# Kernel optimization log

Measured on AMD Instinct MI355X. Metric: run time of the kernel, lower is better.

## Reference

```python
import jax, jax.numpy as jnp
import numpy as np

B, HIST, N, E = 16, 24, 256, 4096
AQI_EM, RNN_H, GNN_H, EDGE_H = 16, 64, 64, 2


def _lstm(x, W_ih, W_hh, b_ih, b_hh):
    # x: [Bn, L, in]; PyTorch LSTM cell, gate order i,f,g,o
    Bn, L, _ = x.shape
    H = W_hh.shape[1]
    xg = jnp.einsum('bli,gi->blg', x, W_ih) + b_ih  # precompute input contributions [Bn,L,4H]

    def step(carry, g_t):
        h, c = carry
        gates = g_t + h @ W_hh.T + b_hh
        i, f, g, o = jnp.split(gates, 4, axis=-1)
        c = jax.nn.sigmoid(f) * c + jax.nn.sigmoid(i) * jnp.tanh(g)
        h = jax.nn.sigmoid(o) * jnp.tanh(c)
        return (h, c), h

    init = (jnp.zeros((Bn, H), x.dtype), jnp.zeros((Bn, H), x.dtype))
    _, hs = jax.lax.scan(step, init, jnp.swapaxes(xg, 0, 1))
    return jnp.swapaxes(hs, 0, 1)  # [Bn,L,H]


def setup_inputs() -> dict:
    key = jax.random.key(0)
    ks = jax.random.split(key, 8)
    return {
        'city_aqi': jax.random.normal(ks[0], (B, HIST, N, 1), jnp.float32),
        'city_conn': jax.random.randint(ks[1], (2, E), 0, N, jnp.int32),
        'city_w': jax.random.normal(ks[2], (E, EDGE_H), jnp.float32),
        'embed_W': jax.random.normal(ks[3], (1, AQI_EM), jnp.float32) * 0.5,
        'embed_b': jnp.zeros((AQI_EM,), jnp.float32),
        'W_ih': jax.random.normal(ks[4], (4 * RNN_H, AQI_EM), jnp.float32) * (1.0 / np.sqrt(RNN_H)),
        'W_hh': jax.random.normal(ks[5], (4 * RNN_H, RNN_H), jnp.float32) * (1.0 / np.sqrt(RNN_H)),
        'b_ih': jnp.zeros((4 * RNN_H,), jnp.float32),
        'b_hh': jnp.zeros((4 * RNN_H,), jnp.float32),
        'mlp1_W': jax.random.normal(ks[6], (2 * RNN_H + EDGE_H, GNN_H), jnp.float32) * (1.0 / np.sqrt(2 * RNN_H + EDGE_H)),
        'mlp1_b': jnp.zeros((GNN_H,), jnp.float32),
        'mlp2_W': jax.random.normal(ks[7], (RNN_H + GNN_H, GNN_H), jnp.float32) * (1.0 / np.sqrt(RNN_H + GNN_H)),
        'mlp2_b': jnp.zeros((GNN_H,), jnp.float32),
        'city_num': N,
    }


def reference(city_aqi, city_conn, city_w, embed_W, embed_b, W_ih, W_hh, b_ih, b_hh, mlp1_W, mlp1_b, mlp2_W, mlp2_b, city_num):
    Bq, L, Nn, _ = city_aqi.shape
    # embedding + LSTM front-end
    x = jnp.transpose(city_aqi, (0, 2, 1, 3))          # [B,N,L,1]
    x = x @ embed_W + embed_b                          # [B,N,L,em]
    x = x.reshape(Bq * Nn, L, -1)
    h = _lstm(x, W_ih, W_hh, b_ih, b_hh)               # [B*N,L,H]
    h = jnp.transpose(h.reshape(Bq, Nn, L, -1), (0, 2, 1, 3))  # [B,L,N,H]
    # batched graph: T = B*L independent graphs with identical edge structure
    T = Bq * L
    x_flat = h.reshape(T * Nn, -1)                     # [T*N,H]
    off = jnp.arange(T, dtype=city_conn.dtype) * jnp.asarray(city_num, city_conn.dtype)
    row = (city_conn[0][None, :] + off[:, None]).reshape(-1)  # [T*E]
    col = (city_conn[1][None, :] + off[:, None]).reshape(-1)
    e = city_conn.shape[1]
    edge_attr = jnp.broadcast_to(city_w[None], (T, e, city_w.shape[1])).reshape(T * e, -1)
    # CityGNN: gather -> concat -> Linear -> scatter_mean -> concat -> Linear
    msg = jnp.concatenate([x_flat[row], x_flat[col], edge_attr], axis=1)
    msg = msg @ mlp1_W + mlp1_b                        # [T*E,gnn_h]
    agg = jax.ops.segment_sum(msg, col, num_segments=T * Nn)
    cnt = jax.ops.segment_sum(jnp.ones((T * e,), msg.dtype), col, num_segments=T * Nn)
    agg = agg / jnp.maximum(cnt, 1.0)[:, None]         # scatter_mean semantics
    out = jnp.concatenate([x_flat, agg], axis=1) @ mlp2_W + mlp2_b
    return out.reshape(-1, L, Nn, out.shape[-1])       # [B,hist_len,N,gnn_h]
```

## Files before the change

### kernel.cpp

```cpp
#include <hip/hip_runtime.h>
#include <hip/hip_bf16.h>

#define B_ 16
#define L_ 24
#define N_ 256
#define E_ 4096
#define T_ (B_ * L_)

constexpr int WP    = 0;
constexpr int WRQ   = WP + 4096;
constexpr int WRM   = WRQ + 4096;
constexpr int WBIAS = WRM + 4096;
constexpr int WALPHA= WBIAS + 16384;
constexpr int WBETA = WALPHA + 256;
constexpr int WDINV = WBETA + 256;
constexpr int WSEL  = WDINV + 256;
constexpr int WSW   = WSEL + 256;
constexpr int WCNTF = WSW + 512;
constexpr int WCOLP = WCNTF + 256;
constexpr int WROWS = WCOLP + 260;
constexpr int WHFRAG= WROWS + 4096;
constexpr int WQFRAG= WHFRAG + 8192;
constexpr int WX    = WQFRAG + 4096;
constexpr int WAFRG = WX + 3145728;

using bf16x8 = __attribute__((ext_vector_type(8))) short;
using f32x4  = __attribute__((ext_vector_type(4))) float;

__device__ __forceinline__ float sigm(float x) { return 1.f / (1.f + __expf(-x)); }
__device__ __forceinline__ float tanh_(float x) { return 2.f / (1.f + __expf(-2.f * x)) - 1.f; }
__device__ __forceinline__ unsigned f2bf(float f) {
    unsigned u = __float_as_uint(f);
    return (u + 0x7fffu + ((u >> 16) & 1u)) >> 16;
}

__global__ __launch_bounds__(256) void k_prep(
    const int* __restrict__ conn, const float* __restrict__ cw,
    const float* __restrict__ Wih, const float* __restrict__ embW,
    const float* __restrict__ embB, const float* __restrict__ bih,
    const float* __restrict__ bhh, const float* __restrict__ Whh,
    const float* __restrict__ m1W, const float* __restrict__ m1b,
    const float* __restrict__ m2W, const float* __restrict__ m2b,
    float* __restrict__ ws) {
    int t = threadIdx.x, blk = blockIdx.x;
    if (blk >= 9) {
        __shared__ unsigned Mw[256 * 64];
        for (int i = t; i < 256 * 64; i += 256) Mw[i] = 0u;
        __syncthreads();
        for (int e = t; e < E_; e += 256) {
            int k = conn[e] & 255;
            int v = conn[E_ + e] & 255;
            atomicAdd(&Mw[v * 64 + (k >> 2)], 1u << ((k & 3) * 8));
        }
        __syncthreads();
        uint4* dst = (uint4*)(ws + WAFRG);
        int base = (blk - 9) * 2048;
        #pragma unroll
        for (int u0 = 0; u0 < 8; ++u0) {
            int u = base + u0 * 256 + t;
            int fi = u >> 6, l = u & 63;
            int nt = fi >> 3, ks = fi & 7;
            int v = nt * 16 + (l & 15);
            int kb = ks * 8 + ((l >> 4) << 1);
            unsigned w0 = Mw[v * 64 + kb];
            unsigned w1 = Mw[v * 64 + kb + 1];
            unsigned uu[4];
            #pragma unroll
            for (int q = 0; q < 2; ++q) {
                unsigned c0 = (w0 >> (q * 16)) & 255u;
                unsigned c1 = (w0 >> (q * 16 + 8)) & 255u;
                uu[q] = f2bf((float)c0) | (f2bf((float)c1) << 16);
                unsigned d0 = (w1 >> (q * 16)) & 255u;
                unsigned d1 = (w1 >> (q * 16 + 8)) & 255u;
                uu[2 + q] = f2bf((float)d0) | (f2bf((float)d1) << 16);
            }
            dst[u] = make_uint4(uu[0], uu[1], uu[2], uu[3]);
        }
        return;
    }
    if (blk >= 5) {
        int idx = (blk - 5) * 256 + t;
        for (int f = idx; f < 2048; f += 1024) {
            int p = f >> 6, l = f & 63;
            int ct = p >> 1, ks = p & 1;
            const float* src = Whh + (ct * 16 + (l & 15)) * 64 + ks * 32 + ((l >> 4) << 3);
            unsigned u[4];
            #pragma unroll
            for (int q = 0; q < 4; ++q)
                u[q] = f2bf(src[2 * q]) | (f2bf(src[2 * q + 1]) << 16);
            ((uint4*)(ws + WHFRAG))[f] = make_uint4(u[0], u[1], u[2], u[3]);
        }
        return;
    }
    if (blk > 0) {
        __shared__ float sB[64 * 64];
        __shared__ float sM[32 * 64];
        int mi = blk - 1;
        bool isP = mi < 2;
        int ks = mi & 1;
        #pragma unroll
        for (int i = 0; i < 16; ++i) sB[t + 256 * i] = m2W[64 * 64 + t + 256 * i];
        __syncthreads();
        int j = t & 63, kl = t >> 6;
        for (int r = 0; r < 8; ++r) {
            int kk = kl * 8 + r;
            int k = ks * 32 + kk;
            const float* arow = m1W + (isP ? k : (64 + k)) * 64;
            float acc = 0.f;
            #pragma unroll
            for (int m = 0; m < 64; m += 4) {
                float4 a4 = *(const float4*)(arow + m);
                acc = fmaf(a4.x, sB[m * 64 + j], acc);
                acc = fmaf(a4.y, sB[(m + 1) * 64 + j], acc);
                acc = fmaf(a4.z, sB[(m + 2) * 64 + j], acc);
                acc = fmaf(a4.w, sB[(m + 3) * 64 + j], acc);
            }
            if (isP) {
                sM[kk * 64 + j] = acc;
            } else {
                ws[WRM + k * 64 + j] = acc;
                sM[kk * 64 + j] = acc + m2W[k * 64 + j];
            }
        }
        __syncthreads();
        {
            int ct = t >> 6, l = t & 63;
            int fi = (isP ? 8 : 0) + ks * 4 + ct;
            int rb = (l >> 4) * 8;
            int n = ct * 16 + (l & 15);
            unsigned uu[4];
            #pragma unroll
            for (int q = 0; q < 4; ++q)
                uu[q] = f2bf(sM[(rb + 2 * q) * 64 + n])
                      | (f2bf(sM[(rb + 2 * q + 1) * 64 + n]) << 16);
            ((uint4*)(ws + WQFRAG))[fi * 64 + l] = make_uint4(uu[0], uu[1], uu[2], uu[3]);
        }
        return;
    }
    __shared__ int s_cnt[N_];
    __shared__ float s_sw0[N_], s_sw1[N_];
    __shared__ float sU[3 * 64];
    s_cnt[t] = 0; s_sw0[t] = 0.f; s_sw1[t] = 0.f;
    __syncthreads();
    for (int e = t; e < E_; e += 256) {
        int c = conn[E_ + e] & 255;
        atomicAdd(&s_cnt[c], 1);
        atomicAdd(&s_sw0[c], cw[2 * e]);
        atomicAdd(&s_sw1[c], cw[2 * e + 1]);
    }
    __syncthreads();
    int cnt = s_cnt[t];
    ws[WCNTF + t] = (float)cnt;
    ws[WDINV + t] = 1.f / (float)(cnt > 1 ? cnt : 1);
    ws[WSEL + t]  = cnt > 0 ? 1.f : 0.f;
    ws[WSW + t]        = s_sw0[t];
    ws[WSW + N_ + t]   = s_sw1[t];
    float a = 0.f, b = 0.f;
    #pragma unroll
    for (int i = 0; i < 16; ++i) {
        float w = Wih[t * 16 + i];
        a += w * embW[i];
        b += w * embB[i];
    }
    ws[WALPHA + t] = a;
    ws[WBETA + t]  = b + bih[t] + bhh[t];
    if (t < 192) {
        int part = t >> 6, j = t & 63;
        float acc = 0.f;
        #pragma unroll 8
        for (int m = 0; m < 64; ++m) {
            float w = (part == 0) ? m1W[128 * 64 + m]
                    : (part == 1) ? m1W[129 * 64 + m] : m1b[m];
            acc = fmaf(w, m2W[(64 + m) * 64 + j], acc);
        }
        sU[part * 64 + j] = acc;
    }
    __syncthreads();
    {
        int j = t & 63;
        float u0 = sU[j], u1 = sU[64 + j], u2 = sU[128 + j];
        float b2j = m2b[j];
        int vb = t >> 6;
        #pragma unroll 8
        for (int i = 0; i < 64; ++i) {
            int v = vb + i * 4;
            int cv = s_cnt[v];
            float dv = 1.f / (float)(cv > 1 ? cv : 1);
            float bb = s_sw0[v] * u0 + s_sw1[v] * u1 + (float)cv * u2;
            ws[WBIAS + v * 64 + j] = dv * bb + b2j;
        }
    }
}

constexpr int HS = 72;

__global__ __launch_bounds__(256, 1) void k_lstm(
    const float* __restrict__ aqi, float* __restrict__ ws) {
    __shared__ __align__(16) short sHhi[2][16 * HS];
    __shared__ __align__(16) short sHlo[2][16 * HS];
    __shared__ float sX[24 * 16];
    int t = threadIdx.x;
    int w = t >> 6, lane = t & 63;
    int seq0 = blockIdx.x * 16;
    int b0 = seq0 >> 8, n0 = seq0 & 255;
    bf16x8 wreg[4][2];
    {
        const bf16x8* wf = (const bf16x8*)(ws + WHFRAG);
        #pragma unroll
        for (int g = 0; g < 4; ++g)
            #pragma unroll
            for (int ks = 0; ks < 2; ++ks)
                wreg[g][ks] = wf[((4 * g + w) * 2 + ks) * 64 + lane];
    }
    for (int i = t; i < 384; i += 256) {
        int l = i >> 4, c = i & 15;
        sX[l * 16 + c] = aqi[(b0 * L_ + l) * N_ + n0 + c];
    }
    unsigned short* xws = (unsigned short*)(ws + WX);
    int c0 = lane & 15, quad = lane >> 4, q4 = quad * 4, q8 = quad * 8;
    float alF[4], beF[4];
    #pragma unroll
    for (int g = 0; g < 4; ++g) {
        alF[g] = ws[WALPHA + (4 * g + w) * 16 + c0];
        beF[g] = ws[WBETA  + (4 * g + w) * 16 + c0];
    }
    float cst[4] = {0.f, 0.f, 0.f, 0.f};
    bf16x8 hA[2][2] = {};
    __syncthreads();
    for (int l = 0; l < L_; ++l) {
        int buf = l & 1;
        f32x4 acc[4];
        #pragma unroll
        for (int g = 0; g < 4; ++g) {
            #pragma unroll
            for (int r = 0; r < 4; ++r)
                acc[g][r] = fmaf(sX[l * 16 + q4 + r], alF[g], beF[g]);
        }
        if (l > 0) {
            #pragma unroll
            for (int g = 0; g < 4; ++g) {
                #pragma unroll
                for (int ks = 0; ks < 2; ++ks) {
                    acc[g] = __builtin_amdgcn_mfma_f32_16x16x32_bf16(
                        hA[0][ks], wreg[g][ks], acc[g], 0, 0, 0);
                    acc[g] = __builtin_amdgcn_mfma_f32_16x16x32_bf16(
                        hA[1][ks], wreg[g][ks], acc[g], 0, 0, 0);
                }
            }
        }
        unsigned short* xrow = xws + ((size_t)(b0 * L_ + l) * N_ + n0) * 64;
        #pragma unroll
        for (int r = 0; r < 4; ++r) {
            float iv = sigm(acc[0][r]);
            float fv = sigm(acc[1][r]);
            float gv = tanh_(acc[2][r]);
            float ov = sigm(acc[3][r]);
            cst[r] = fmaf(fv, cst[r], iv * gv);
            float h = ov * tanh_(cst[r]);
            unsigned hb = f2bf(h);
            xrow[(q4 + r) * 64 + w * 16 + c0] = (unsigned short)hb;
            float hf = __uint_as_float(hb << 16);
            unsigned lb = f2bf(h - hf);
            sHhi[buf][(q4 + r) * HS + w * 16 + c0] = (short)hb;
            sHlo[buf][(q4 + r) * HS + w * 16 + c0] = (short)lb;
        }
        __syncthreads();
        hA[0][0] = *(const bf16x8*)&sHhi[buf][c0 * HS + q8];
        hA[0][1] = *(const bf16x8*)&sHhi[buf][c0 * HS + 32 + q8];
        hA[1][0] = *(const bf16x8*)&sHlo[buf][c0 * HS + q8];
        hA[1][1] = *(const bf16x8*)&sHlo[buf][c0 * HS + 32 + q8];
    }
}

constexpr int XS = 72;

__global__ __launch_bounds__(256, 2) void k_graph(
    const float* __restrict__ ws, float* __restrict__ out) {
    __shared__ __align__(16) short Xl[N_ * XS];
    __shared__ __align__(16) short Sl[N_ * XS];
    int tg = blockIdx.x;
    int tid = threadIdx.x;
    int lane = tid & 63, w = tid >> 6;
    int c0 = lane & 15, quad = lane >> 4, q8 = quad * 8;
    const uint4* src = (const uint4*)((const unsigned short*)(ws + WX)
                                      + (size_t)tg * (N_ * 64));
    #pragma unroll
    for (int it = 0; it < 8; ++it) {
        int idx = tid + it * 256;
        uint4 d = src[idx];
        int node = idx >> 3, q = idx & 7;
        *(uint4*)&Xl[node * XS + q * 8] = d;
    }
    float dv[16];
    #pragma unroll
    for (int nt = 0; nt < 16; ++nt) dv[nt] = ws[WDINV + nt * 16 + c0];
    __syncthreads();
    bf16x8 af[8];
    {
        int colb = w * 16 + (c0 & 14);
        int sh = (c0 & 1) * 16;
        int rbase = (lane >> 4) * 8;
        #pragma unroll
        for (int ks = 0; ks < 8; ++ks) {
            unsigned wd[8];
            #pragma unroll
            for (int j = 0; j < 8; ++j)
                wd[j] = *(const unsigned*)&Xl[(ks * 32 + rbase + j) * XS + colb];
            union { bf16x8 v; unsigned u[4]; } tmp;
            #pragma unroll
            for (int q = 0; q < 4; ++q)
                tmp.u[q] = ((wd[2 * q] >> sh) & 0xffffu)
                         | (((wd[2 * q + 1] >> sh) & 0xffffu) << 16);
            af[ks] = tmp.v;
        }
    }
    f32x4 acc[16];
    #pragma unroll
    for (int nt = 0; nt < 16; ++nt) {
        #pragma unroll
        for (int r = 0; r < 4; ++r) acc[nt][r] = 0.f;
    }
    {
        const bf16x8* bsrc = (const bf16x8*)(ws + WAFRG);
        #pragma unroll
        for (int nt = 0; nt < 16; ++nt) {
            bf16x8 bf[8];
            #pragma unroll
            for (int ks = 0; ks < 8; ++ks)
                bf[ks] = bsrc[(nt * 8 + ks) * 64 + lane];
            #pragma unroll
            for (int ks = 0; ks < 8; ++ks)
                acc[nt] = __builtin_amdgcn_mfma_f32_16x16x32_bf16(
                    af[ks], bf[ks], acc[nt], 0, 0, 0);
        }
    }
    {
        int j0 = w * 16 + quad * 4;
        #pragma unroll
        for (int nt = 0; nt < 16; ++nt) {
            float d = dv[nt];
            unsigned p0 = f2bf(acc[nt][0] * d) | (f2bf(acc[nt][1] * d) << 16);
            unsigned p1 = f2bf(acc[nt][2] * d) | (f2bf(acc[nt][3] * d) << 16);
            int v = nt * 16 + c0;
            *(uint2*)&Sl[v * XS + j0] = make_uint2(p0, p1);
        }
    }
    __syncthreads();
    bf16x8 bq[16];
    {
        const bf16x8* qf = (const bf16x8*)(ws + WQFRAG);
        #pragma unroll
        for (int i = 0; i < 16; ++i) bq[i] = qf[i * 64 + lane];
    }
    const float* bias = ws + WBIAS;
    #pragma unroll
    for (int rti = 0; rti < 4; ++rti) {
        int rt = w * 4 + rti;
        const short* xr = &Xl[(rt * 16 + c0) * XS];
        const short* sr = &Sl[(rt * 16 + c0) * XS];
        bf16x8 ax0 = *(const bf16x8*)(xr + q8);
        bf16x8 ax1 = *(const bf16x8*)(xr + 32 + q8);
        bf16x8 as0 = *(const bf16x8*)(sr + q8);
        bf16x8 as1 = *(const bf16x8*)(sr + 32 + q8);
        #pragma unroll
        for (int ct = 0; ct < 4; ++ct) {
            f32x4 a2;
            #pragma unroll
            for (int r = 0; r < 4; ++r)
                a2[r] = bias[(rt * 16 + quad * 4 + r) * 64 + ct * 16 + c0];
            a2 = __builtin_amdgcn_mfma_f32_16x16x32_bf16(ax0, bq[ct],      a2, 0, 0, 0);
            a2 = __builtin_amdgcn_mfma_f32_16x16x32_bf16(ax1, bq[4 + ct],  a2, 0, 0, 0);
            a2 = __builtin_amdgcn_mfma_f32_16x16x32_bf16(as0, bq[8 + ct],  a2, 0, 0, 0);
            a2 = __builtin_amdgcn_mfma_f32_16x16x32_bf16(as1, bq[12 + ct], a2, 0, 0, 0);
            #pragma unroll
            for (int r = 0; r < 4; ++r)
                out[((size_t)tg * 256 + rt * 16 + quad * 4 + r) * 64 + ct * 16 + c0]
                    = a2[r];
        }
    }
    int v = tid;
    float sel = ws[WSEL + v];
    if (__syncthreads_or(sel < 0.5f)) {
        if (sel < 0.5f) {
            float* og = out + ((size_t)tg * 256 + v) * 64;
            #pragma unroll
            for (int jc = 0; jc < 4; ++jc) {
                float corr[16];
                #pragma unroll
                for (int j = 0; j < 16; ++j) corr[j] = 0.f;
                #pragma unroll
                for (int k = 0; k < 64; ++k) {
                    unsigned hv = (unsigned short)Xl[v * XS + k];
                    float xk = __uint_as_float(hv << 16);
                    const float* Q = ws + WRM + k * 64 + jc * 16;
                    #pragma unroll
                    for (int j = 0; j < 16; ++j) corr[j] += xk * Q[j];
                }
                #pragma unroll
                for (int j = 0; j < 16; ++j) og[jc * 16 + j] -= corr[j];
            }
        }
    }
}

extern "C" void kernel_launch(void* const* d_in, const int* in_sizes, int n_in,
                              void* d_out, int out_size, void* d_ws, size_t ws_size,
                              hipStream_t stream) {
    const float* aqi  = (const float*)d_in[0];
    const int*   conn = (const int*)d_in[1];
    const float* cw   = (const float*)d_in[2];
    const float* embW = (const float*)d_in[3];
    const float* embB = (const float*)d_in[4];
    const float* Wih  = (const float*)d_in[5];
    const float* Whh  = (const float*)d_in[6];
    const float* bih  = (const float*)d_in[7];
    const float* bhh  = (const float*)d_in[8];
    const float* m1W  = (const float*)d_in[9];
    const float* m1b  = (const float*)d_in[10];
    const float* m2W  = (const float*)d_in[11];
    const float* m2b  = (const float*)d_in[12];
    float* ws  = (float*)d_ws;
    float* out = (float*)d_out;

    k_prep<<<dim3(13), dim3(256), 0, stream>>>(conn, cw, Wih, embW, embB, bih, bhh,
                                               Whh, m1W, m1b, m2W, m2b, ws);
    k_lstm<<<dim3(256), dim3(256), 0, stream>>>(aqi, ws);
    k_graph<<<dim3(T_), dim3(256), 0, stream>>>(ws, out);
}
```

Measured before the change: 158.7 us.

## Merge prep and LSTM kernels into one launch with per-block W_hh conversion

The prep kernel and the LSTM kernel become one launch. Blocks 0-255 run the LSTM and each converts W_hh to bf16 fragments and computes the embedding-folded input weights itself. Blocks 256+ do the graph-side precomputation. This removes a kernel launch and the serial dependency between prep and the LSTM. It also batches each step's global h stores into contiguous 8-byte writes from shared memory. In exchange every LSTM block repeats the weight conversion, and the kernel now reserves 64KB of shared memory for all blocks.

```diff
diff --git a/kernel.cpp b/kernel.cpp
--- a/kernel.cpp
+++ b/kernel.cpp
@@ -34,17 +34,115 @@
     return (u + 0x7fffu + ((u >> 16) & 1u)) >> 16;
 }
 
-__global__ __launch_bounds__(256) void k_prep(
-    const int* __restrict__ conn, const float* __restrict__ cw,
-    const float* __restrict__ Wih, const float* __restrict__ embW,
-    const float* __restrict__ embB, const float* __restrict__ bih,
-    const float* __restrict__ bhh, const float* __restrict__ Whh,
-    const float* __restrict__ m1W, const float* __restrict__ m1b,
-    const float* __restrict__ m2W, const float* __restrict__ m2b,
-    float* __restrict__ ws) {
+constexpr int HS = 72;
+
+__global__ __launch_bounds__(256, 2) void k_main(
+    const float* __restrict__ aqi, const int* __restrict__ conn,
+    const float* __restrict__ cw, const float* __restrict__ Wih,
+    const float* __restrict__ embW, const float* __restrict__ embB,
+    const float* __restrict__ bih, const float* __restrict__ bhh,
+    const float* __restrict__ Whh, const float* __restrict__ m1W,
+    const float* __restrict__ m1b, const float* __restrict__ m2W,
+    const float* __restrict__ m2b, float* __restrict__ ws) {
+    __shared__ __align__(16) char smem[65536];
     int t = threadIdx.x, blk = blockIdx.x;
-    if (blk >= 9) {
-        __shared__ unsigned Mw[256 * 64];
+
+    if (blk >= 256) {
+        int role = blk - 256;
+        if (role == 0) {
+            int* s_cnt   = (int*)smem;
+            float* s_sw0 = (float*)(smem + 1024);
+            float* s_sw1 = (float*)(smem + 2048);
+            float* sU    = (float*)(smem + 3072);
+            s_cnt[t] = 0; s_sw0[t] = 0.f; s_sw1[t] = 0.f;
+            __syncthreads();
+            for (int e = t; e < E_; e += 256) {
+                int c = conn[E_ + e] & 255;
+                atomicAdd(&s_cnt[c], 1);
+                atomicAdd(&s_sw0[c], cw[2 * e]);
+                atomicAdd(&s_sw1[c], cw[2 * e + 1]);
+            }
+            __syncthreads();
+            int cnt = s_cnt[t];
+            ws[WCNTF + t] = (float)cnt;
+            ws[WDINV + t] = 1.f / (float)(cnt > 1 ? cnt : 1);
+            ws[WSEL + t]  = cnt > 0 ? 1.f : 0.f;
+            ws[WSW + t]        = s_sw0[t];
+            ws[WSW + N_ + t]   = s_sw1[t];
+            if (t < 192) {
+                int part = t >> 6, j = t & 63;
+                float acc = 0.f;
+                #pragma unroll 8
+                for (int m = 0; m < 64; ++m) {
+                    float w = (part == 0) ? m1W[128 * 64 + m]
+                            : (part == 1) ? m1W[129 * 64 + m] : m1b[m];
+                    acc = fmaf(w, m2W[(64 + m) * 64 + j], acc);
+                }
+                sU[part * 64 + j] = acc;
+            }
+            __syncthreads();
+            {
+                int j = t & 63;
+                float u0 = sU[j], u1 = sU[64 + j], u2 = sU[128 + j];
+                float b2j = m2b[j];
+                int vb = t >> 6;
+                #pragma unroll 8
+                for (int i = 0; i < 64; ++i) {
+                    int v = vb + i * 4;
+                    int cv = s_cnt[v];
+                    float dv = 1.f / (float)(cv > 1 ? cv : 1);
+                    float bb = s_sw0[v] * u0 + s_sw1[v] * u1 + (float)cv * u2;
+                    ws[WBIAS + v * 64 + j] = dv * bb + b2j;
+                }
+            }
+            return;
+        }
+        if (role <= 4) {
+            float* sB = (float*)smem;
+            float* sM = (float*)(smem + 16384);
+            int mi = role - 1;
+            bool isP = mi < 2;
+            int ks = mi & 1;
+            #pragma unroll
+            for (int i = 0; i < 16; ++i) sB[t + 256 * i] = m2W[64 * 64 + t + 256 * i];
+            __syncthreads();
+            int j = t & 63, kl = t >> 6;
+            for (int r = 0; r < 8; ++r) {
+                int kk = kl * 8 + r;
+                int k = ks * 32 + kk;
+                const float* arow = m1W + (isP ? k : (64 + k)) * 64;
+                float acc = 0.f;
+                #pragma unroll
+                for (int m = 0; m < 64; m += 4) {
+                    float4 a4 = *(const float4*)(arow + m);
+                    acc = fmaf(a4.x, sB[m * 64 + j], acc);
+                    acc = fmaf(a4.y, sB[(m + 1) * 64 + j], acc);
+                    acc = fmaf(a4.z, sB[(m + 2) * 64 + j], acc);
+                    acc = fmaf(a4.w, sB[(m + 3) * 64 + j], acc);
+                }
+                if (isP) {
+                    sM[kk * 64 + j] = acc;
+                } else {
+                    ws[WRM + k * 64 + j] = acc;
+                    sM[kk * 64 + j] = acc + m2W[k * 64 + j];
+                }
+            }
+            __syncthreads();
+            {
+                int ct = t >> 6, l = t & 63;
+                int fi = (isP ? 8 : 0) + ks * 4 + ct;
+                int rb = (l >> 4) * 8;
+                int n = ct * 16 + (l & 15);
+                unsigned uu[4];
+                #pragma unroll
+                for (int q = 0; q < 4; ++q)
+                    uu[q] = f2bf(sM[(rb + 2 * q) * 64 + n])
+                          | (f2bf(sM[(rb + 2 * q + 1) * 64 + n]) << 16);
+                ((uint4*)(ws + WQFRAG))[fi * 64 + l] = make_uint4(uu[0], uu[1], uu[2], uu[3]);
+            }
+            return;
+        }
+        unsigned* Mw = (unsigned*)smem;
         for (int i = t; i < 256 * 64; i += 256) Mw[i] = 0u;
         __syncthreads();
         for (int e = t; e < E_; e += 256) {
@@ -54,7 +152,7 @@
         }
         __syncthreads();
         uint4* dst = (uint4*)(ws + WAFRG);
-        int base = (blk - 9) * 2048;
+        int base = (role - 5) * 2048;
         #pragma unroll
         for (int u0 = 0; u0 < 8; ++u0) {
             int u = base + u0 * 256 + t;
@@ -78,152 +176,47 @@
         }
         return;
     }
-    if (blk >= 5) {
-        int idx = (blk - 5) * 256 + t;
-        for (int f = idx; f < 2048; f += 1024) {
-            int p = f >> 6, l = f & 63;
-            int ct = p >> 1, ks = p & 1;
-            const float* src = Whh + (ct * 16 + (l & 15)) * 64 + ks * 32 + ((l >> 4) << 3);
-            unsigned u[4];
+
+    short* sHhi = (short*)smem;
+    short* sHlo = (short*)(smem + 4608);
+    float* sX   = (float*)(smem + 9216);
+    int w = t >> 6, lane = t & 63;
+    int seq0 = blk * 16;
+    int b0 = seq0 >> 8, n0 = seq0 & 255;
+    int c0 = lane & 15, quad = lane >> 4, q4 = quad * 4, q8 = quad * 8;
+    bf16x8 wreg[4][2];
+    #pragma unroll
+    for (int g = 0; g < 4; ++g) {
+        int ct = 4 * g + w;
+        #pragma unroll
+        for (int ks = 0; ks < 2; ++ks) {
+            const float* src = Whh + (ct * 16 + c0) * 64 + ks * 32 + q8;
+            union { bf16x8 v; unsigned u[4]; } tmp;
             #pragma unroll
             for (int q = 0; q < 4; ++q)
-                u[q] = f2bf(src[2 * q]) | (f2bf(src[2 * q + 1]) << 16);
-            ((uint4*)(ws + WHFRAG))[f] = make_uint4(u[0], u[1], u[2], u[3]);
-        }
-        return;
-    }
-    if (blk > 0) {
-        __shared__ float sB[64 * 64];
-        __shared__ float sM[32 * 64];
-        int mi = blk - 1;
-        bool isP = mi < 2;
-        int ks = mi & 1;
-        #pragma unroll
-        for (int i = 0; i < 16; ++i) sB[t + 256 * i] = m2W[64 * 64 + t + 256 * i];
-        __syncthreads();
-        int j = t & 63, kl = t >> 6;
-        for (int r = 0; r < 8; ++r) {
-            int kk = kl * 8 + r;
-            int k = ks * 32 + kk;
-            const float* arow = m1W + (isP ? k : (64 + k)) * 64;
-            float acc = 0.f;
-            #pragma unroll
-            for (int m = 0; m < 64; m += 4) {
-                float4 a4 = *(const float4*)(arow + m);
-                acc = fmaf(a4.x, sB[m * 64 + j], acc);
-                acc = fmaf(a4.y, sB[(m + 1) * 64 + j], acc);
-                acc = fmaf(a4.z, sB[(m + 2) * 64 + j], acc);
-                acc = fmaf(a4.w, sB[(m + 3) * 64 + j], acc);
-            }
-            if (isP) {
-                sM[kk * 64 + j] = acc;
-            } else {
-                ws[WRM + k * 64 + j] = acc;
-                sM[kk * 64 + j] = acc + m2W[k * 64 + j];
-            }
-        }
-        __syncthreads();
-        {
-            int ct = t >> 6, l = t & 63;
-            int fi = (isP ? 8 : 0) + ks * 4 + ct;
-            int rb = (l >> 4) * 8;
-            int n = ct * 16 + (l & 15);
-            unsigned uu[4];
-            #pragma unroll
-            for (int q = 0; q < 4; ++q)
-                uu[q] = f2bf(sM[(rb + 2 * q) * 64 + n])
-                      | (f2bf(sM[(rb + 2 * q + 1) * 64 + n]) << 16);
-            ((uint4*)(ws + WQFRAG))[fi * 64 + l] = make_uint4(uu[0], uu[1], uu[2], uu[3]);
-        }
-        return;
-    }
-    __shared__ int s_cnt[N_];
-    __shared__ float s_sw0[N_], s_sw1[N_];
-    __shared__ float sU[3 * 64];
-    s_cnt[t] = 0; s_sw0[t] = 0.f; s_sw1[t] = 0.f;
-    __syncthreads();
-    for (int e = t; e < E_; e += 256) {
-        int c = conn[E_ + e] & 255;
-        atomicAdd(&s_cnt[c], 1);
-        atomicAdd(&s_sw0[c], cw[2 * e]);
-        atomicAdd(&s_sw1[c], cw[2 * e + 1]);
-    }
-    __syncthreads();
-    int cnt = s_cnt[t];
-    ws[WCNTF + t] = (float)cnt;
-    ws[WDINV + t] = 1.f / (float)(cnt > 1 ? cnt : 1);
-    ws[WSEL + t]  = cnt > 0 ? 1.f : 0.f;
-    ws[WSW + t]        = s_sw0[t];
-    ws[WSW + N_ + t]   = s_sw1[t];
-    float a = 0.f, b = 0.f;
-    #pragma unroll
-    for (int i = 0; i < 16; ++i) {
-        float w = Wih[t * 16 + i];
-        a += w * embW[i];
-        b += w * embB[i];
-    }
-    ws[WALPHA + t] = a;
-    ws[WBETA + t]  = b + bih[t] + bhh[t];
-    if (t < 192) {
-        int part = t >> 6, j = t & 63;
-        float acc = 0.f;
-        #pragma unroll 8
-        for (int m = 0; m < 64; ++m) {
-            float w = (part == 0) ? m1W[128 * 64 + m]
-                    : (part == 1) ? m1W[129 * 64 + m] : m1b[m];
-            acc = fmaf(w, m2W[(64 + m) * 64 + j], acc);
-        }
-        sU[part * 64 + j] = acc;
-    }
-    __syncthreads();
-    {
-        int j = t & 63;
-        float u0 = sU[j], u1 = sU[64 + j], u2 = sU[128 + j];
-        float b2j = m2b[j];
-        int vb = t >> 6;
-        #pragma unroll 8
-        for (int i = 0; i < 64; ++i) {
-            int v = vb + i * 4;
-            int cv = s_cnt[v];
-            float dv = 1.f / (float)(cv > 1 ? cv : 1);
-            float bb = s_sw0[v] * u0 + s_sw1[v] * u1 + (float)cv * u2;
-            ws[WBIAS + v * 64 + j] = dv * bb + b2j;
-        }
-    }
-}
-
-constexpr int HS = 72;
-
-__global__ __launch_bounds__(256, 1) void k_lstm(
-    const float* __restrict__ aqi, float* __restrict__ ws) {
-    __shared__ __align__(16) short sHhi[2][16 * HS];
-    __shared__ __align__(16) short sHlo[2][16 * HS];
-    __shared__ float sX[24 * 16];
-    int t = threadIdx.x;
-    int w = t >> 6, lane = t & 63;
-    int seq0 = blockIdx.x * 16;
-    int b0 = seq0 >> 8, n0 = seq0 & 255;
-    bf16x8 wreg[4][2];
-    {
-        const bf16x8* wf = (const bf16x8*)(ws + WHFRAG);
-        #pragma unroll
-        for (int g = 0; g < 4; ++g)
-            #pragma unroll
-            for (int ks = 0; ks < 2; ++ks)
-                wreg[g][ks] = wf[((4 * g + w) * 2 + ks) * 64 + lane];
+                tmp.u[q] = f2bf(src[2 * q]) | (f2bf(src[2 * q + 1]) << 16);
+            wreg[g][ks] = tmp.v;
+        }
     }
     for (int i = t; i < 384; i += 256) {
         int l = i >> 4, c = i & 15;
         sX[l * 16 + c] = aqi[(b0 * L_ + l) * N_ + n0 + c];
     }
+    float alF[4], beF[4];
+    #pragma unroll
+    for (int g = 0; g < 4; ++g) {
+        int tp = (4 * g + w) * 16 + c0;
+        float a = 0.f, b = 0.f;
+        #pragma unroll
+        for (int i = 0; i < 16; ++i) {
+            float wv = Wih[tp * 16 + i];
+            a += wv * embW[i];
+            b += wv * embB[i];
+        }
+        alF[g] = a;
+        beF[g] = b + bih[tp] + bhh[tp];
+    }
     unsigned short* xws = (unsigned short*)(ws + WX);
-    int c0 = lane & 15, quad = lane >> 4, q4 = quad * 4, q8 = quad * 8;
-    float alF[4], beF[4];
-    #pragma unroll
-    for (int g = 0; g < 4; ++g) {
-        alF[g] = ws[WALPHA + (4 * g + w) * 16 + c0];
-        beF[g] = ws[WBETA  + (4 * g + w) * 16 + c0];
-    }
     float cst[4] = {0.f, 0.f, 0.f, 0.f};
     bf16x8 hA[2][2] = {};
     __syncthreads();
@@ -248,7 +241,6 @@
                 }
             }
         }
-        unsigned short* xrow = xws + ((size_t)(b0 * L_ + l) * N_ + n0) * 64;
         #pragma unroll
         for (int r = 0; r < 4; ++r) {
             float iv = sigm(acc[0][r]);
@@ -258,17 +250,21 @@
             cst[r] = fmaf(fv, cst[r], iv * gv);
             float h = ov * tanh_(cst[r]);
             unsigned hb = f2bf(h);
-            xrow[(q4 + r) * 64 + w * 16 + c0] = (unsigned short)hb;
             float hf = __uint_as_float(hb << 16);
             unsigned lb = f2bf(h - hf);
-            sHhi[buf][(q4 + r) * HS + w * 16 + c0] = (short)hb;
-            sHlo[buf][(q4 + r) * HS + w * 16 + c0] = (short)lb;
+            sHhi[buf * (16 * HS) + (q4 + r) * HS + w * 16 + c0] = (short)hb;
+            sHlo[buf * (16 * HS) + (q4 + r) * HS + w * 16 + c0] = (short)lb;
         }
         __syncthreads();
-        hA[0][0] = *(const bf16x8*)&sHhi[buf][c0 * HS + q8];
-        hA[0][1] = *(const bf16x8*)&sHhi[buf][c0 * HS + 32 + q8];
-        hA[1][0] = *(const bf16x8*)&sHlo[buf][c0 * HS + q8];
-        hA[1][1] = *(const bf16x8*)&sHlo[buf][c0 * HS + 32 + q8];
+        hA[0][0] = *(const bf16x8*)&sHhi[buf * (16 * HS) + c0 * HS + q8];
+        hA[0][1] = *(const bf16x8*)&sHhi[buf * (16 * HS) + c0 * HS + 32 + q8];
+        hA[1][0] = *(const bf16x8*)&sHlo[buf * (16 * HS) + c0 * HS + q8];
+        hA[1][1] = *(const bf16x8*)&sHlo[buf * (16 * HS) + c0 * HS + 32 + q8];
+        {
+            int row = t >> 4, ch = t & 15;
+            uint2 xa = *(const uint2*)&sHhi[buf * (16 * HS) + row * HS + ch * 4];
+            *(uint2*)(xws + ((size_t)(b0 * L_ + l) * N_ + n0) * 64 + row * 64 + ch * 4) = xa;
+        }
     }
 }
 
@@ -422,8 +418,8 @@
     float* ws  = (float*)d_ws;
     float* out = (float*)d_out;
 
-    k_prep<<<dim3(13), dim3(256), 0, stream>>>(conn, cw, Wih, embW, embB, bih, bhh,
-                                               Whh, m1W, m1b, m2W, m2b, ws);
-    k_lstm<<<dim3(256), dim3(256), 0, stream>>>(aqi, ws);
+    k_main<<<dim3(265), dim3(256), 0, stream>>>(aqi, conn, cw, Wih, embW, embB,
+                                                bih, bhh, Whh, m1W, m1b, m2W,
+                                                m2b, ws);
     k_graph<<<dim3(T_), dim3(256), 0, stream>>>(ws, out);
 }
```

Result: faster. 142.6 us (-10.2%).
